# Kernel tuning notes

Measured on AMD Instinct MI355X. Metric: run time of the kernel, lower is better.

The kernel has to match this reference:

```python
import jax, jax.numpy as jnp
import numpy as np

G, N, E, F, C, H = 2, 20000, 160000, 128, 64, 8
NEG_SLOPE = 0.2


def setup_inputs() -> dict:
    key = jax.random.key(0)
    ks = jax.random.split(key, 16)
    def w(k, shape, fan_in):
        return jax.random.normal(k, shape, jnp.float32) * (1.0 / np.sqrt(fan_in))
    z = lambda *s: jnp.zeros(s, jnp.float32)
    return {
        "x": jax.random.normal(ks[0], (G, N, F), jnp.float32),
        "edge_index": jax.random.randint(ks[1], (G, 2, E), 0, N, jnp.int32),
        "edge_weight": jax.random.uniform(ks[2], (G, E), jnp.float32),
        "Wl1": w(ks[3], (F, H * C), F), "bl1": z(H * C),
        "Wr1": w(ks[4], (F, H * C), F), "br1": z(H * C),
        "We1": w(ks[5], (1, H * C), 1),
        "att1": w(ks[6], (H, C), C),
        "bias1": z(H * C),
        "Wl2": w(ks[7], (H * C, C), H * C), "bl2": z(C),
        "Wr2": w(ks[8], (H * C, C), H * C), "br2": z(C),
        "We2": w(ks[9], (1, C), 1),
        "att2": w(ks[10], (1, C), C),
        "bias2": z(C),
        "Wg": w(ks[11], (C, C), C), "bg": z(C),
        "Wn": w(ks[12], (2 * C, C), 2 * C), "bn": z(C),
        "Wo": w(ks[13], (C, 1), C), "bo": z(1),
    }


def _segment_softmax(logits, seg, n):
    m = jax.ops.segment_max(logits, seg, num_segments=n)
    ex = jnp.exp(logits - m[seg])
    den = jax.ops.segment_sum(ex, seg, num_segments=n)
    return ex / den[seg]


def _gatv2(x, src, dst, eattr, Wl, bl, Wr, br, We, att, bias, heads, concat):
    # Faithful PyG GATv2Conv (share_weights=False, edge_dim=1).
    n = x.shape[0]
    hc = Wl.shape[1]
    c = hc // heads
    xl = (x @ Wl + bl).reshape(n, heads, c)   # lin_l (source / message)
    xr = (x @ Wr + br).reshape(n, heads, c)   # lin_r (target)
    ee = (eattr @ We).reshape(-1, heads, c)   # lin_edge (bias=False)
    s = jax.nn.leaky_relu(xl[src] + xr[dst] + ee, NEG_SLOPE)  # [Etot, H, C]
    logit = jnp.einsum('ehc,hc->eh', s, att)
    alpha = _segment_softmax(logit, dst, n)   # softmax over incoming edges
    out = jax.ops.segment_sum(alpha[..., None] * xl[src], dst, num_segments=n)
    out = out.reshape(n, hc) if concat else out.mean(axis=1)
    return out + bias


def _forward(edge_index, x, edge_weight, Wl1, bl1, Wr1, br1, We1, att1, bias1,
             Wl2, bl2, Wr2, br2, We2, att2, bias2, Wg, bg, Wn, bn, Wo, bo):
    n = x.shape[1]
    def per_graph(xg, eig, ewg):
        src, dst = eig[0], eig[1]
        ea = ewg[:, None]  # edge_weight.unsqueeze(-1), edge_dim=1
        # add_self_loops with fill_value='mean' (mean of edge_attr grouped by dst)
        cnt = jax.ops.segment_sum(jnp.ones_like(ewg), dst, num_segments=n)
        loop = jax.ops.segment_sum(ea, dst, num_segments=n) / jnp.clip(cnt, 1.0)[:, None]
        ar = jnp.arange(n, dtype=src.dtype)
        src2 = jnp.concatenate([src, ar])
        dst2 = jnp.concatenate([dst, ar])
        ea2 = jnp.concatenate([ea, loop], axis=0)
        h = jax.nn.elu(_gatv2(xg, src2, dst2, ea2, Wl1, bl1, Wr1, br1, We1, att1, bias1, H, True))
        h = jax.nn.elu(_gatv2(h, src2, dst2, ea2, Wl2, bl2, Wr2, br2, We2, att2, bias2, 1, False))
        return h
    h = jax.vmap(per_graph)(x, edge_index, edge_weight)      # [G, N, C]
    g_emb = h.max(axis=1)                                    # global_max_pool per graph
    Gv = g_emb.max(axis=0)                                   # max over graphs -> [C]
    Gv = jax.nn.relu(Gv @ Wg + bg)
    Hc = jnp.concatenate([h, jnp.broadcast_to(Gv, h.shape)], axis=-1)  # [G,N,2C]
    h2 = jax.nn.relu(Hc @ Wn + bn)
    return (h2 @ Wo + bo)[..., 0]                            # [G, N] logits


def reference(x, edge_index, edge_weight, Wl1, bl1, Wr1, br1, We1, att1, bias1,
              Wl2, bl2, Wr2, br2, We2, att2, bias2, Wg, bg, Wn, bn, Wo, bo):
    return _forward(edge_index, x, edge_weight, Wl1, bl1, Wr1, br1, We1, att1, bias1,
                    Wl2, bl2, Wr2, br2, We2, att2, bias2, Wg, bg, Wn, bn, Wo, bo)
```

## Files before the change

### kernel.cpp

```cpp
#include <hip/hip_runtime.h>
#include <hip/hip_bf16.h>
#include <cstdint>
#include <cstddef>

#define NEG_SLOPE 0.2f

static constexpr int Gg = 2;
static constexpr int Nn = 20000;
static constexpr int Ee = 160000;
static constexpr int Ff = 128;
static constexpr int Cc = 64;
static constexpr int HC = 512;
static constexpr int GN = Gg * Nn;
static constexpr int GNP = 40064;
static constexpr int DEGMAX = 48;

typedef __attribute__((ext_vector_type(8))) short short8;
typedef __attribute__((ext_vector_type(4))) float floatx4;

__device__ __forceinline__ float bf2f(unsigned short b) {
    return __uint_as_float(((unsigned)b) << 16);
}
__device__ __forceinline__ unsigned short f2bf(float x) {
    unsigned u = __float_as_uint(x);
    unsigned r = 0x7fffu + ((u >> 16) & 1u);
    return (unsigned short)((u + r) >> 16);
}
__device__ __forceinline__ void unpack8(const uint4 p, float* f) {
    f[0] = __uint_as_float(p.x << 16); f[1] = __uint_as_float(p.x & 0xffff0000u);
    f[2] = __uint_as_float(p.y << 16); f[3] = __uint_as_float(p.y & 0xffff0000u);
    f[4] = __uint_as_float(p.z << 16); f[5] = __uint_as_float(p.z & 0xffff0000u);
    f[6] = __uint_as_float(p.w << 16); f[7] = __uint_as_float(p.w & 0xffff0000u);
}
__device__ __forceinline__ void unpack4(const uint2 p, float* f) {
    f[0] = __uint_as_float(p.x << 16); f[1] = __uint_as_float(p.x & 0xffff0000u);
    f[2] = __uint_as_float(p.y << 16); f[3] = __uint_as_float(p.y & 0xffff0000u);
}
__device__ __forceinline__ unsigned encf(float x) {
    unsigned u = __float_as_uint(x);
    return (u & 0x80000000u) ? ~u : (u | 0x80000000u);
}
__device__ __forceinline__ float decf(unsigned e) {
    return __uint_as_float((e & 0x80000000u) ? (e ^ 0x80000000u) : ~e);
}

__global__ void castprep_k(const float* __restrict__ x, unsigned short* __restrict__ xb,
                           const float* __restrict__ Wl1, const float* __restrict__ Wr1,
                           const float* __restrict__ bl1, const float* __restrict__ br1,
                           const float* __restrict__ Wl2, const float* __restrict__ Wr2,
                           const float* __restrict__ bl2, const float* __restrict__ br2,
                           unsigned short* __restrict__ Wt1, unsigned short* __restrict__ Wt2,
                           float* __restrict__ b1cat, float* __restrict__ b2cat,
                           int* __restrict__ cnt, unsigned* __restrict__ gmax) {
    int t = blockIdx.x * 256 + threadIdx.x;
    size_t base = (size_t)t * 4;
    if (base < (size_t)GNP * Ff) {
        ushort4 ov;
        if (base < (size_t)GN * Ff) {
            float4 v = *(const float4*)(x + base);
            ov.x = f2bf(v.x); ov.y = f2bf(v.y); ov.z = f2bf(v.z); ov.w = f2bf(v.w);
        } else {
            ov.x = ov.y = ov.z = ov.w = 0;
        }
        *(ushort4*)(xb + base) = ov;
    }
    if (t < 1024 * 128) {
        int n = t >> 7, k = t & 127;
        float v = (n < 512) ? Wl1[(size_t)k * 512 + n] : Wr1[(size_t)k * 512 + n - 512];
        Wt1[t] = f2bf(v);
    }
    if (t < 128 * 512) {
        int n = t >> 9, k = t & 511;
        float v = (n < 64) ? Wl2[(size_t)k * 64 + n] : Wr2[(size_t)k * 64 + n - 64];
        Wt2[t] = f2bf(v);
    }
    if (t < 1024) b1cat[t] = (t < 512) ? bl1[t] : br1[t - 512];
    if (t < 128)  b2cat[t] = (t < 64) ? bl2[t] : br2[t - 64];
    if (t < GN)   cnt[t] = 0;
    if (t < 1024) gmax[t] = 0u;
}

template <int K, bool EDGES>
__global__ __launch_bounds__(256) void mfma_gemm_k(const unsigned short* __restrict__ A, int lda,
                                                   const unsigned short* __restrict__ Bt,
                                                   const float* __restrict__ bias,
                                                   unsigned short* __restrict__ Cg, int ldc,
                                                   int Mreal,
                                                   const int* __restrict__ ei,
                                                   const float* __restrict__ ew,
                                                   int* __restrict__ cnt,
                                                   int2* __restrict__ sedge) {
    if (EDGES) {
        int bid = blockIdx.y * gridDim.x + blockIdx.x;
        int idx = bid * 256 + threadIdx.x;
        if (idx < Gg * Ee) {
            int g = (idx >= Ee) ? 1 : 0;
            int e = idx - g * Ee;
            int src = ei[(size_t)g * 2 * Ee + e];
            int dst = ei[(size_t)g * 2 * Ee + Ee + e];
            float wv = ew[idx];
            int node = g * Nn + dst;
            int pos = atomicAdd(&cnt[node], 1);
            if (pos < DEGMAX) {
                int2 v; v.x = src; v.y = __float_as_int(wv);
                sedge[(size_t)node * DEGMAX + pos] = v;
            }
        }
    }

    __shared__ unsigned short As[128 * 32];
    __shared__ unsigned short Bs[128 * 32];
    const int t = threadIdx.x;
    const int lane = t & 63;
    const int wid = t >> 6;
    const int wm = wid >> 1, wn = wid & 1;
    const int m0 = blockIdx.x * 128;
    const int n0 = blockIdx.y * 128;

    floatx4 acc[4][4] = {};

    const int jrow = t >> 2;
    const int js = t & 3;
    const int wavebase = (t & 192) * 16;

    for (int k0 = 0; k0 < K; k0 += 32) {
#pragma unroll
        for (int r = 0; r < 2; ++r) {
            int row = jrow + r * 64;
            int c = js ^ ((row >> 1) & 3);
            const unsigned short* gA = A + (size_t)(m0 + row) * lda + k0 + c * 8;
            const unsigned short* gB = Bt + (size_t)(n0 + row) * K + k0 + c * 8;
            __builtin_amdgcn_global_load_lds(
                (const __attribute__((address_space(1))) void*)gA,
                (__attribute__((address_space(3))) void*)((char*)As + r * 4096 + wavebase),
                16, 0, 0);
            __builtin_amdgcn_global_load_lds(
                (const __attribute__((address_space(1))) void*)gB,
                (__attribute__((address_space(3))) void*)((char*)Bs + r * 4096 + wavebase),
                16, 0, 0);
        }
        __syncthreads();

        const int lrow = lane & 15, lc = lane >> 4;
        short8 af[4], bf[4];
#pragma unroll
        for (int i2 = 0; i2 < 4; ++i2) {
            int rA = wm * 64 + i2 * 16 + lrow;
            int sA = lc ^ ((rA >> 1) & 3);
            af[i2] = *(const short8*)((const char*)As + (rA * 4 + sA) * 16);
        }
#pragma unroll
        for (int j2 = 0; j2 < 4; ++j2) {
            int rB = wn * 64 + j2 * 16 + lrow;
            int sB = lc ^ ((rB >> 1) & 3);
            bf[j2] = *(const short8*)((const char*)Bs + (rB * 4 + sB) * 16);
        }
#pragma unroll
        for (int i2 = 0; i2 < 4; ++i2)
#pragma unroll
            for (int j2 = 0; j2 < 4; ++j2)
                acc[i2][j2] = __builtin_amdgcn_mfma_f32_16x16x32_bf16(bf[j2], af[i2], acc[i2][j2], 0, 0, 0);
        __syncthreads();
    }

    const int mrow = m0 + wm * 64 + (lane & 15);
    const int ncol0 = n0 + wn * 64 + ((lane >> 4) << 2);
    float4 bq[4];
#pragma unroll
    for (int j2 = 0; j2 < 4; ++j2) bq[j2] = *(const float4*)(bias + ncol0 + j2 * 16);
#pragma unroll
    for (int i2 = 0; i2 < 4; ++i2) {
        int m = mrow + i2 * 16;
        if (m < Mreal) {
#pragma unroll
            for (int j2 = 0; j2 < 4; ++j2) {
                ushort4 ov;
                ov.x = f2bf(acc[i2][j2][0] + bq[j2].x);
                ov.y = f2bf(acc[i2][j2][1] + bq[j2].y);
                ov.z = f2bf(acc[i2][j2][2] + bq[j2].z);
                ov.w = f2bf(acc[i2][j2][3] + bq[j2].w);
                *(ushort4*)(Cg + (size_t)m * ldc + ncol0 + j2 * 16) = ov;
            }
        }
    }
}

__global__ __launch_bounds__(256) void agg1_k(const unsigned short* xlr,
                                              const int2* __restrict__ sedge,
                                              const int* __restrict__ cnt,
                                              const float* __restrict__ att1, const float* __restrict__ We1,
                                              const float* __restrict__ bias1,
                                              unsigned short* h1, float* __restrict__ loopw) {
    const int lane = threadIdx.x & 63;
    const int node = (blockIdx.x << 2) + (threadIdx.x >> 6);
    if (node >= GN) return;
    const int g = (node >= Nn) ? 1 : 0;

    float attv[8], wev[8];
    {
        float4 a0 = *(const float4*)(att1 + lane * 8);
        float4 a1 = *(const float4*)(att1 + lane * 8 + 4);
        attv[0] = a0.x; attv[1] = a0.y; attv[2] = a0.z; attv[3] = a0.w;
        attv[4] = a1.x; attv[5] = a1.y; attv[6] = a1.z; attv[7] = a1.w;
        float4 w0 = *(const float4*)(We1 + lane * 8);
        float4 w1 = *(const float4*)(We1 + lane * 8 + 4);
        wev[0] = w0.x; wev[1] = w0.y; wev[2] = w0.z; wev[3] = w0.w;
        wev[4] = w1.x; wev[5] = w1.y; wev[6] = w1.z; wev[7] = w1.w;
    }
    float xrv[8];
    unpack8(((const uint4*)(xlr + (size_t)node * 1024 + 512))[lane], xrv);

    const int ec = cnt[node];
    const int2* ep = sedge + (size_t)node * DEGMAX;
    const uint4* rowb = (const uint4*)(xlr + (size_t)g * Nn * 1024) + lane;

    float lsum = 0.f, wsum = 0.f;
    float acc[8] = {};

    uint4 r0, r1; int2 s0v, s1v;
    if (ec > 0) { s0v = ep[0]; r0 = rowb[(size_t)s0v.x * 128]; }
    if (ec > 1) { s1v = ep[1]; r1 = rowb[(size_t)s1v.x * 128]; }
    int e = 0;
    while (e + 1 < ec) {
        uint4 r2, r3; int2 s2v, s3v;
        if (e + 2 < ec) { s2v = ep[e + 2]; r2 = rowb[(size_t)s2v.x * 128]; }
        if (e + 3 < ec) { s3v = ep[e + 3]; r3 = rowb[(size_t)s3v.x * 128]; }
        float xa[8], xb_[8];
        unpack8(r0, xa);
        unpack8(r1, xb_);
        float wa = __int_as_float(s0v.y), wb = __int_as_float(s1v.y);
        wsum += wa + wb;
        float ta = 0.f, tb = 0.f;
#pragma unroll
        for (int j = 0; j < 8; ++j) {
            float sa = xa[j] + fmaf(wa, wev[j], xrv[j]);
            float sb = xb_[j] + fmaf(wb, wev[j], xrv[j]);
            sa = fmaxf(sa, NEG_SLOPE * sa);
            sb = fmaxf(sb, NEG_SLOPE * sb);
            ta = fmaf(sa, attv[j], ta);
            tb = fmaf(sb, attv[j], tb);
        }
        ta += __shfl_xor(ta, 1); tb += __shfl_xor(tb, 1);
        ta += __shfl_xor(ta, 2); tb += __shfl_xor(tb, 2);
        ta += __shfl_xor(ta, 4); tb += __shfl_xor(tb, 4);
        float pa = __expf(ta), pb = __expf(tb);
        lsum += pa + pb;
#pragma unroll
        for (int j = 0; j < 8; ++j) acc[j] = fmaf(pa, xa[j], fmaf(pb, xb_[j], acc[j]));
        r0 = r2; s0v = s2v; r1 = r3; s1v = s3v;
        e += 2;
    }
    if (e < ec) {
        float xa[8];
        unpack8(r0, xa);
        float wa = __int_as_float(s0v.y);
        wsum += wa;
        float ta = 0.f;
#pragma unroll
        for (int j = 0; j < 8; ++j) {
            float sa = xa[j] + fmaf(wa, wev[j], xrv[j]);
            sa = fmaxf(sa, NEG_SLOPE * sa);
            ta = fmaf(sa, attv[j], ta);
        }
        ta += __shfl_xor(ta, 1); ta += __shfl_xor(ta, 2); ta += __shfl_xor(ta, 4);
        float pa = __expf(ta);
        lsum += pa;
#pragma unroll
        for (int j = 0; j < 8; ++j) acc[j] = fmaf(pa, xa[j], acc[j]);
    }

    float lw = wsum / fmaxf((float)ec, 1.f);
    {
        float xv[8];
        unpack8(((const uint4*)(xlr + (size_t)node * 1024))[lane], xv);
        float tp = 0.f;
#pragma unroll
        for (int j = 0; j < 8; ++j) {
            float s = xv[j] + fmaf(lw, wev[j], xrv[j]);
            s = fmaxf(s, NEG_SLOPE * s);
            tp = fmaf(s, attv[j], tp);
        }
        tp += __shfl_xor(tp, 1); tp += __shfl_xor(tp, 2); tp += __shfl_xor(tp, 4);
        float p = __expf(tp);
        lsum += p;
#pragma unroll
        for (int j = 0; j < 8; ++j) acc[j] = fmaf(p, xv[j], acc[j]);
    }

    float inv = 1.f / lsum;
    float4 b0 = *(const float4*)(bias1 + lane * 8);
    float4 b1 = *(const float4*)(bias1 + lane * 8 + 4);
    float bvv[8] = {b0.x, b0.y, b0.z, b0.w, b1.x, b1.y, b1.z, b1.w};
    float ov[8];
#pragma unroll
    for (int j = 0; j < 8; ++j) {
        float o = fmaf(acc[j], inv, bvv[j]);
        ov[j] = o > 0.f ? o : (__expf(o) - 1.f);
    }
    uint4 pk;
    pk.x = (unsigned)f2bf(ov[0]) | ((unsigned)f2bf(ov[1]) << 16);
    pk.y = (unsigned)f2bf(ov[2]) | ((unsigned)f2bf(ov[3]) << 16);
    pk.z = (unsigned)f2bf(ov[4]) | ((unsigned)f2bf(ov[5]) << 16);
    pk.w = (unsigned)f2bf(ov[6]) | ((unsigned)f2bf(ov[7]) << 16);
    ((uint4*)(h1 + (size_t)node * 1024))[lane] = pk;
    if (lane == 0) loopw[node] = lw;
}

__global__ __launch_bounds__(256) void agg2_k(const unsigned short* __restrict__ xlr2,
                                              const int2* __restrict__ sedge,
                                              const int* __restrict__ cnt,
                                              const float* __restrict__ loopw,
                                              const float* __restrict__ att2, const float* __restrict__ We2,
                                              const float* __restrict__ bias2,
                                              float* __restrict__ hout, unsigned* __restrict__ gmax) {
    const int tid = threadIdx.x;
    const int lane = tid & 63;
    const int cs = lane & 15;
    const int sub = lane >> 4;
    const int w4 = (blockIdx.x << 2) + (tid >> 6);
    const int node = w4 * 4 + sub;
    const int g = (node >= Nn) ? 1 : 0;

    float4 av = *(const float4*)(att2 + cs * 4);
    float4 wv4 = *(const float4*)(We2 + cs * 4);
    float attv[4] = {av.x, av.y, av.z, av.w};
    float wevv[4] = {wv4.x, wv4.y, wv4.z, wv4.w};
    float xrv[4];
    unpack4(*(const uint2*)(xlr2 + (size_t)node * 128 + 64 + cs * 4), xrv);
    const unsigned short* rowb = xlr2 + (size_t)g * Nn * 128;

    float lsum, acc[4];
    {
        float lw = loopw[node];
        float xv[4];
        unpack4(*(const uint2*)(xlr2 + (size_t)node * 128 + cs * 4), xv);
        float tp = 0.f;
#pragma unroll
        for (int j = 0; j < 4; ++j) {
            float s = xv[j] + fmaf(lw, wevv[j], xrv[j]);
            s = fmaxf(s, NEG_SLOPE * s);
            tp = fmaf(s, attv[j], tp);
        }
        tp += __shfl_xor(tp, 1); tp += __shfl_xor(tp, 2);
        tp += __shfl_xor(tp, 4); tp += __shfl_xor(tp, 8);
        float p = __expf(tp);
        lsum = p;
#pragma unroll
        for (int j = 0; j < 4; ++j) acc[j] = p * xv[j];
    }

    const int ec = cnt[node];
    const int2* ep = sedge + (size_t)node * DEGMAX;

    uint2 r0 = {0, 0}, r1 = {0, 0};
    int2 s0v = {0, 0}, s1v = {0, 0};
    if (0 < ec) { s0v = ep[0]; r0 = *(const uint2*)(rowb + (size_t)s0v.x * 128 + cs * 4); }
    if (1 < ec) { s1v = ep[1]; r1 = *(const uint2*)(rowb + (size_t)s1v.x * 128 + cs * 4); }
    int e = 0;
    while (__any(e < ec)) {
        uint2 r2 = {0, 0}, r3 = {0, 0};
        int2 s2v = {0, 0}, s3v = {0, 0};
        if (e + 2 < ec) { s2v = ep[e + 2]; r2 = *(const uint2*)(rowb + (size_t)s2v.x * 128 + cs * 4); }
        if (e + 3 < ec) { s3v = ep[e + 3]; r3 = *(const uint2*)(rowb + (size_t)s3v.x * 128 + cs * 4); }
        bool v0 = (e < ec), v1 = (e + 1 < ec);
        float xa[4], xb_[4];
        unpack4(r0, xa);
        unpack4(r1, xb_);
        float wa = __int_as_float(s0v.y), wb = __int_as_float(s1v.y);
        float ta = 0.f, tb = 0.f;
#pragma unroll
        for (int j = 0; j < 4; ++j) {
            float sa = xa[j] + fmaf(wa, wevv[j], xrv[j]);
            float sb = xb_[j] + fmaf(wb, wevv[j], xrv[j]);
            sa = fmaxf(sa, NEG_SLOPE * sa);
            sb = fmaxf(sb, NEG_SLOPE * sb);
            ta = fmaf(sa, attv[j], ta);
            tb = fmaf(sb, attv[j], tb);
        }
        ta += __shfl_xor(ta, 1); tb += __shfl_xor(tb, 1);
        ta += __shfl_xor(ta, 2); tb += __shfl_xor(tb, 2);
        ta += __shfl_xor(ta, 4); tb += __shfl_xor(tb, 4);
        ta += __shfl_xor(ta, 8); tb += __shfl_xor(tb, 8);
        float pa = v0 ? __expf(ta) : 0.f;
        float pb = v1 ? __expf(tb) : 0.f;
        lsum += pa + pb;
#pragma unroll
        for (int j = 0; j < 4; ++j) acc[j] = fmaf(pa, xa[j], fmaf(pb, xb_[j], acc[j]));
        r0 = r2; s0v = s2v; r1 = r3; s1v = s3v;
        e += 2;
    }

    float inv = 1.f / lsum;
    float4 bv = *(const float4*)(bias2 + cs * 4);
    float bvv[4] = {bv.x, bv.y, bv.z, bv.w};
    float ov[4];
#pragma unroll
    for (int j = 0; j < 4; ++j) {
        float o = fmaf(acc[j], inv, bvv[j]);
        ov[j] = o > 0.f ? o : (__expf(o) - 1.f);
    }
    float4 o4;
    o4.x = ov[0]; o4.y = ov[1]; o4.z = ov[2]; o4.w = ov[3];
    *(float4*)(hout + (size_t)node * Cc + cs * 4) = o4;

    float mj[4];
#pragma unroll
    for (int j = 0; j < 4; ++j) {
        float m = ov[j];
        m = fmaxf(m, __shfl_xor(m, 16));
        m = fmaxf(m, __shfl_xor(m, 32));
        mj[j] = m;
    }
    __shared__ unsigned bm[64];
    if (tid < 64) bm[tid] = 0u;
    __syncthreads();
    if (sub == 0) {
#pragma unroll
        for (int j = 0; j < 4; ++j) atomicMax(&bm[cs * 4 + j], encf(mj[j]));
    }
    __syncthreads();
    if (tid < 64) atomicMax(&gmax[tid * 16], bm[tid]);
}

__global__ __launch_bounds__(256) void final_k(const float* __restrict__ h,
                                               const unsigned* __restrict__ gmax,
                                               const float* __restrict__ Wg, const float* __restrict__ bg,
                                               const float* __restrict__ Wn, const float* __restrict__ bn,
                                               const float* __restrict__ Wo, const float* __restrict__ bo,
                                               float* __restrict__ out) {
    __shared__ float wns[64 * 64];
    __shared__ float g0s[64], g1s[64], cvs[64];
    const int tid = threadIdx.x;
    for (int k = tid; k < 64 * 64; k += 256) wns[k] = Wn[k];
    if (tid < 64) g0s[tid] = decf(gmax[tid * 16]);
    __syncthreads();
    if (tid < 64) {
        float a = bg[tid];
        for (int c = 0; c < 64; ++c) a += g0s[c] * Wg[c * 64 + tid];
        g1s[tid] = fmaxf(a, 0.f);
    }
    __syncthreads();
    if (tid < 64) {
        float b = bn[tid];
        for (int c = 0; c < 64; ++c) b += g1s[c] * Wn[(64 + c) * 64 + tid];
        cvs[tid] = b;
    }
    __syncthreads();

    const int lane = tid & 63;
    const int cs = lane & 15;
    const int sub = lane >> 4;
    const int node = blockIdx.x * 16 + (tid >> 6) * 4 + sub;

    float4 h4 = *(const float4*)(h + (size_t)node * Cc + cs * 4);
    float hv[4] = {h4.x, h4.y, h4.z, h4.w};
    float inner[4] = {cvs[cs * 4 + 0], cvs[cs * 4 + 1], cvs[cs * 4 + 2], cvs[cs * 4 + 3]};
#pragma unroll
    for (int c = 0; c < 64; ++c) {
        float hc = __shfl(hv[c & 3], sub * 16 + (c >> 2));
        float4 wv = *(const float4*)&wns[c * 64 + cs * 4];
        inner[0] = fmaf(hc, wv.x, inner[0]);
        inner[1] = fmaf(hc, wv.y, inner[1]);
        inner[2] = fmaf(hc, wv.z, inner[2]);
        inner[3] = fmaf(hc, wv.w, inner[3]);
    }
    float4 wo4 = *(const float4*)(Wo + cs * 4);
    float woa[4] = {wo4.x, wo4.y, wo4.z, wo4.w};
    float t = 0.f;
#pragma unroll
    for (int j = 0; j < 4; ++j) {
        float v = fmaxf(inner[j], 0.f);
        t = fmaf(v, woa[j], t);
    }
    t += __shfl_xor(t, 1); t += __shfl_xor(t, 2);
    t += __shfl_xor(t, 4); t += __shfl_xor(t, 8);
    if (cs == 0) out[node] = t + bo[0];
}

extern "C" void kernel_launch(void* const* d_in, const int* in_sizes, int n_in,
                              void* d_out, int out_size, void* d_ws, size_t ws_size,
                              hipStream_t stream) {
    const float* x     = (const float*)d_in[0];
    const int*   ei    = (const int*)d_in[1];
    const float* ew    = (const float*)d_in[2];
    const float* Wl1   = (const float*)d_in[3];
    const float* bl1v  = (const float*)d_in[4];
    const float* Wr1   = (const float*)d_in[5];
    const float* br1v  = (const float*)d_in[6];
    const float* We1   = (const float*)d_in[7];
    const float* att1  = (const float*)d_in[8];
    const float* bias1 = (const float*)d_in[9];
    const float* Wl2   = (const float*)d_in[10];
    const float* bl2v  = (const float*)d_in[11];
    const float* Wr2   = (const float*)d_in[12];
    const float* br2v  = (const float*)d_in[13];
    const float* We2   = (const float*)d_in[14];
    const float* att2  = (const float*)d_in[15];
    const float* bias2 = (const float*)d_in[16];
    const float* Wg    = (const float*)d_in[17];
    const float* bgv   = (const float*)d_in[18];
    const float* Wn    = (const float*)d_in[19];
    const float* bnv   = (const float*)d_in[20];
    const float* Wo    = (const float*)d_in[21];
    const float* bov   = (const float*)d_in[22];
    float* out = (float*)d_out;

    char* w = (char*)d_ws;
    size_t o = 0;
    auto take = [&](size_t b) -> char* {
        char* p = w + o;
        o += (b + 255) & ~(size_t)255;
        return p;
    };
    unsigned short* xlr1 = (unsigned short*)take((size_t)GNP * 1024 * 2);
    unsigned short* xb   = (unsigned short*)take((size_t)GNP * Ff * 2);
    unsigned short* xlr2 = (unsigned short*)take((size_t)GNP * 128 * 2);
    unsigned short* Wt1  = (unsigned short*)take(1024 * 128 * 2);
    unsigned short* Wt2  = (unsigned short*)take(128 * 512 * 2);
    float* b1cat = (float*)take(1024 * 4);
    float* b2cat = (float*)take(128 * 4);
    int*    cnt   = (int*)take((size_t)GN * 4);
    float*  loopw = (float*)take((size_t)GN * 4);
    int2*   sedge = (int2*)take((size_t)GN * DEGMAX * 8);
    unsigned* gmax = (unsigned*)take(1024 * 4);
    unsigned short* h1 = xlr1 + 512;
    float* hbuf = (float*)xb;

    castprep_k<<<((GNP * Ff / 4) + 255) / 256, 256, 0, stream>>>(
        x, xb, Wl1, Wr1, bl1v, br1v, Wl2, Wr2, bl2v, br2v, Wt1, Wt2, b1cat, b2cat, cnt, gmax);

    mfma_gemm_k<Ff, true><<<dim3(GNP / 128, 8), 256, 0, stream>>>(
        xb, Ff, Wt1, b1cat, xlr1, 1024, GN, ei, ew, cnt, sedge);

    agg1_k<<<GN / 4, 256, 0, stream>>>(xlr1, sedge, cnt, att1, We1, bias1, h1, loopw);

    mfma_gemm_k<HC, false><<<dim3(GNP / 128, 1), 256, 0, stream>>>(
        h1, 1024, Wt2, b2cat, xlr2, 128, GN, nullptr, nullptr, nullptr, nullptr);

    agg2_k<<<GN / 16, 256, 0, stream>>>(xlr2, sedge, cnt, loopw, att2, We2, bias2, hbuf, gmax);

    final_k<<<GN / 16, 256, 0, stream>>>(hbuf, gmax, Wg, bgv, Wn, bnv, Wo, bov, out);

    (void)in_sizes; (void)n_in; (void)out_size; (void)ws_size;
}
```

Before: 336.2 us.

## Split agg2 edge list across four 16-lane groups per node wavefront

```diff
diff --git a/kernel.cpp b/kernel.cpp
--- a/kernel.cpp
+++ b/kernel.cpp
@@ -306,19 +306,18 @@
     if (lane == 0) loopw[node] = lw;
 }
 
-__global__ __launch_bounds__(256) void agg2_k(const unsigned short* __restrict__ xlr2,
-                                              const int2* __restrict__ sedge,
-                                              const int* __restrict__ cnt,
-                                              const float* __restrict__ loopw,
-                                              const float* __restrict__ att2, const float* __restrict__ We2,
-                                              const float* __restrict__ bias2,
-                                              float* __restrict__ hout, unsigned* __restrict__ gmax) {
+__global__ __launch_bounds__(1024) void agg2_k(const unsigned short* __restrict__ xlr2,
+                                               const int2* __restrict__ sedge,
+                                               const int* __restrict__ cnt,
+                                               const float* __restrict__ loopw,
+                                               const float* __restrict__ att2, const float* __restrict__ We2,
+                                               const float* __restrict__ bias2,
+                                               float* __restrict__ hout, unsigned* __restrict__ gmax) {
     const int tid = threadIdx.x;
     const int lane = tid & 63;
     const int cs = lane & 15;
     const int sub = lane >> 4;
-    const int w4 = (blockIdx.x << 2) + (tid >> 6);
-    const int node = w4 * 4 + sub;
+    const int node = blockIdx.x * 16 + (tid >> 6);
     const int g = (node >= Nn) ? 1 : 0;
 
     float4 av = *(const float4*)(att2 + cs * 4);
@@ -329,40 +328,23 @@
     unpack4(*(const uint2*)(xlr2 + (size_t)node * 128 + 64 + cs * 4), xrv);
     const unsigned short* rowb = xlr2 + (size_t)g * Nn * 128;
 
-    float lsum, acc[4];
-    {
-        float lw = loopw[node];
-        float xv[4];
-        unpack4(*(const uint2*)(xlr2 + (size_t)node * 128 + cs * 4), xv);
-        float tp = 0.f;
-#pragma unroll
-        for (int j = 0; j < 4; ++j) {
-            float s = xv[j] + fmaf(lw, wevv[j], xrv[j]);
-            s = fmaxf(s, NEG_SLOPE * s);
-            tp = fmaf(s, attv[j], tp);
-        }
-        tp += __shfl_xor(tp, 1); tp += __shfl_xor(tp, 2);
-        tp += __shfl_xor(tp, 4); tp += __shfl_xor(tp, 8);
-        float p = __expf(tp);
-        lsum = p;
-#pragma unroll
-        for (int j = 0; j < 4; ++j) acc[j] = p * xv[j];
-    }
-
     const int ec = cnt[node];
     const int2* ep = sedge + (size_t)node * DEGMAX;
-
+    const int lo = (ec * sub) >> 2;
+    const int hi = (ec * (sub + 1)) >> 2;
+
+    float lsum = 0.f, acc[4] = {};
+
+    int e = lo;
     uint2 r0 = {0, 0}, r1 = {0, 0};
     int2 s0v = {0, 0}, s1v = {0, 0};
-    if (0 < ec) { s0v = ep[0]; r0 = *(const uint2*)(rowb + (size_t)s0v.x * 128 + cs * 4); }
-    if (1 < ec) { s1v = ep[1]; r1 = *(const uint2*)(rowb + (size_t)s1v.x * 128 + cs * 4); }
-    int e = 0;
-    while (__any(e < ec)) {
+    if (e < hi)     { s0v = ep[e];     r0 = *(const uint2*)(rowb + (size_t)s0v.x * 128 + cs * 4); }
+    if (e + 1 < hi) { s1v = ep[e + 1]; r1 = *(const uint2*)(rowb + (size_t)s1v.x * 128 + cs * 4); }
+    while (e + 1 < hi) {
         uint2 r2 = {0, 0}, r3 = {0, 0};
         int2 s2v = {0, 0}, s3v = {0, 0};
-        if (e + 2 < ec) { s2v = ep[e + 2]; r2 = *(const uint2*)(rowb + (size_t)s2v.x * 128 + cs * 4); }
-        if (e + 3 < ec) { s3v = ep[e + 3]; r3 = *(const uint2*)(rowb + (size_t)s3v.x * 128 + cs * 4); }
-        bool v0 = (e < ec), v1 = (e + 1 < ec);
+        if (e + 2 < hi) { s2v = ep[e + 2]; r2 = *(const uint2*)(rowb + (size_t)s2v.x * 128 + cs * 4); }
+        if (e + 3 < hi) { s3v = ep[e + 3]; r3 = *(const uint2*)(rowb + (size_t)s3v.x * 128 + cs * 4); }
         float xa[4], xb_[4];
         unpack4(r0, xa);
         unpack4(r1, xb_);
@@ -381,13 +363,56 @@
         ta += __shfl_xor(ta, 2); tb += __shfl_xor(tb, 2);
         ta += __shfl_xor(ta, 4); tb += __shfl_xor(tb, 4);
         ta += __shfl_xor(ta, 8); tb += __shfl_xor(tb, 8);
-        float pa = v0 ? __expf(ta) : 0.f;
-        float pb = v1 ? __expf(tb) : 0.f;
+        float pa = __expf(ta), pb = __expf(tb);
         lsum += pa + pb;
 #pragma unroll
         for (int j = 0; j < 4; ++j) acc[j] = fmaf(pa, xa[j], fmaf(pb, xb_[j], acc[j]));
         r0 = r2; s0v = s2v; r1 = r3; s1v = s3v;
         e += 2;
+    }
+    if (e < hi) {
+        float xa[4];
+        unpack4(r0, xa);
+        float wa = __int_as_float(s0v.y);
+        float ta = 0.f;
+#pragma unroll
+        for (int j = 0; j < 4; ++j) {
+            float sa = xa[j] + fmaf(wa, wevv[j], xrv[j]);
+            sa = fmaxf(sa, NEG_SLOPE * sa);
+            ta = fmaf(sa, attv[j], ta);
+        }
+        ta += __shfl_xor(ta, 1); ta += __shfl_xor(ta, 2);
+        ta += __shfl_xor(ta, 4); ta += __shfl_xor(ta, 8);
+        float pa = __expf(ta);
+        lsum += pa;
+#pragma unroll
+        for (int j = 0; j < 4; ++j) acc[j] = fmaf(pa, xa[j], acc[j]);
+    }
+
+    lsum += __shfl_xor(lsum, 16); lsum += __shfl_xor(lsum, 32);
+#pragma unroll
+    for (int j = 0; j < 4; ++j) {
+        acc[j] += __shfl_xor(acc[j], 16);
+        acc[j] += __shfl_xor(acc[j], 32);
+    }
+
+    {
+        float lw = loopw[node];
+        float xv[4];
+        unpack4(*(const uint2*)(xlr2 + (size_t)node * 128 + cs * 4), xv);
+        float tp = 0.f;
+#pragma unroll
+        for (int j = 0; j < 4; ++j) {
+            float s = xv[j] + fmaf(lw, wevv[j], xrv[j]);
+            s = fmaxf(s, NEG_SLOPE * s);
+            tp = fmaf(s, attv[j], tp);
+        }
+        tp += __shfl_xor(tp, 1); tp += __shfl_xor(tp, 2);
+        tp += __shfl_xor(tp, 4); tp += __shfl_xor(tp, 8);
+        float p = __expf(tp);
+        lsum += p;
+#pragma unroll
+        for (int j = 0; j < 4; ++j) acc[j] = fmaf(p, xv[j], acc[j]);
     }
 
     float inv = 1.f / lsum;
@@ -399,24 +424,18 @@
         float o = fmaf(acc[j], inv, bvv[j]);
         ov[j] = o > 0.f ? o : (__expf(o) - 1.f);
     }
-    float4 o4;
-    o4.x = ov[0]; o4.y = ov[1]; o4.z = ov[2]; o4.w = ov[3];
-    *(float4*)(hout + (size_t)node * Cc + cs * 4) = o4;
-
-    float mj[4];
-#pragma unroll
-    for (int j = 0; j < 4; ++j) {
-        float m = ov[j];
-        m = fmaxf(m, __shfl_xor(m, 16));
-        m = fmaxf(m, __shfl_xor(m, 32));
-        mj[j] = m;
-    }
+    if (sub == 0) {
+        float4 o4;
+        o4.x = ov[0]; o4.y = ov[1]; o4.z = ov[2]; o4.w = ov[3];
+        *(float4*)(hout + (size_t)node * Cc + cs * 4) = o4;
+    }
+
     __shared__ unsigned bm[64];
     if (tid < 64) bm[tid] = 0u;
     __syncthreads();
     if (sub == 0) {
 #pragma unroll
-        for (int j = 0; j < 4; ++j) atomicMax(&bm[cs * 4 + j], encf(mj[j]));
+        for (int j = 0; j < 4; ++j) atomicMax(&bm[cs * 4 + j], encf(ov[j]));
     }
     __syncthreads();
     if (tid < 64) atomicMax(&gmax[tid * 16], bm[tid]);
@@ -537,7 +556,7 @@
     mfma_gemm_k<HC, false><<<dim3(GNP / 128, 1), 256, 0, stream>>>(
         h1, 1024, Wt2, b2cat, xlr2, 128, GN, nullptr, nullptr, nullptr, nullptr);
 
-    agg2_k<<<GN / 16, 256, 0, stream>>>(xlr2, sedge, cnt, loopw, att2, We2, bias2, hbuf, gmax);
+    agg2_k<<<GN / 16, 1024, 0, stream>>>(xlr2, sedge, cnt, loopw, att2, We2, bias2, hbuf, gmax);
 
     final_k<<<GN / 16, 256, 0, stream>>>(hbuf, gmax, Wg, bgv, Wn, bnv, Wo, bov, out);
 
```

Result: no change. 330.8 us (-1.6%).
